# Kernel optimization log

Hardware: AMD Instinct MI355X
Metric: run time of the kernel (lower is better)

Reference implementation:

```python
import jax, jax.numpy as jnp
import numpy as np

N_X = 3
NE = 2048
Emin = 1.0
Emax = 100.0


def setup_inputs() -> dict:
    key = jax.random.key(0)
    k1, k2, k3, k4 = jax.random.split(key, 4)
    # log-spaced energy grid (MeV); code assumes E_grid[0] == Emin
    E_grid = jnp.logspace(np.log10(Emin), np.log10(Emax), NE, dtype=jnp.float32)
    # rates O(1), kernels small -> diagonally dominant per-step system, stable recursion
    R = 1.0 + jax.random.uniform(k1, (N_X, NE), dtype=jnp.float32)
    K = 1e-3 * jax.random.uniform(k2, (N_X, N_X, NE, NE), dtype=jnp.float32)
    S0 = jax.random.uniform(k3, (N_X,), dtype=jnp.float32)
    SC = jax.random.uniform(k4, (N_X, NE), dtype=jnp.float32)
    T = jnp.float32(0.01)
    return {"E_grid": E_grid, "R": R, "K": K, "S0": S0, "SC": SC, "T": T}


def _solve_cascade(E_grid, R, K, S0, SC, T):
    n_x, ne = R.shape
    dy = jnp.log(E_grid[-1] / Emin) / (ne - 1)

    src_last = S0 / R[:, -1]  # (N_X,) : S0[Xp] / R[Xp, -1]
    # boundary value at highest energy: FX_E0[X] = SC[X,-1]/R[X,-1] + sum_Xp K[X,Xp,-1,-1]*S0[Xp]/(R[Xp,-1]*R[X,-1])
    FX_E0 = SC[:, -1] / R[:, -1] + (K[:, :, -1, -1] @ src_last) / R[:, -1]
    F0 = jnp.zeros((n_x, ne), dtype=E_grid.dtype).at[:, -1].set(FX_E0)

    jidx = jnp.arange(ne)

    def step(F, i):
        Ki = K[:, :, i, :]  # (N_X, N_X, NE) slice at outer grid point i
        # trapezoid weights over j: dy*E[j] for i < j < NE-1, half-weight at j = NE-1, 0 elsewhere
        w = jnp.where((jidx > i) & (jidx < ne - 1), dy * E_grid, jnp.zeros((), E_grid.dtype))
        w = w.at[-1].set(0.5 * dy * E_grid[-1])
        # a[X] = SC[X,i] + sum_Xp,j Ki[X,Xp,j] * w[j] * F[Xp,j] + sum_Xp Ki[X,Xp,-1]*S0[Xp]/R[Xp,-1]
        a = SC[:, i] + jnp.einsum('xpj,pj->x', Ki, w * F) + Ki[:, :, -1] @ src_last
        # B[X,Xp] = -0.5*dy*E[i]*K[X,Xp,i,i] + R[X,i]*delta(X,Xp)
        B = -0.5 * dy * E_grid[i] * Ki[:, :, i] + jnp.diag(R[:, i])
        F = F.at[:, i].set(jnp.linalg.solve(B, a))
        return F, None

    idx = jnp.arange(ne - 2, -1, -1)  # backward sweep i = NE-2 ... 0
    F_grid, _ = jax.lax.scan(step, F0, idx)

    approx_zero = jnp.asarray(1e-200, F_grid.dtype)  # underflows to 0 in fp32, matching clamp intent
    F_grid = jnp.where(F_grid > approx_zero, F_grid, approx_zero)

    # sol: row 0 = E_grid, rows 1..N_X = spectra
    return jnp.concatenate([E_grid[None, :], F_grid], axis=0)


def reference(E_grid, R, K, S0, SC, T):
    return _solve_cascade(E_grid, R, K, S0, SC, T)
```

## Files before the change

### kernel.cpp

```cpp
#include <hip/hip_runtime.h>
#include <cstddef>
#include <cstdint>

#define NE 2048
#define NX 3
#define NROWS (NE - 1)
#define BS 64
#define BR (3 * BS)
#define NBLK 32
#define NPAIR 16


static __device__ __forceinline__ float dy_of(const float* E) {
    return logf(E[NE - 1] / E[0]) / (float)(NE - 1);
}

#define DOT4(a, b) ((a).x * (b).x + (a).y * (b).y + (a).z * (b).z + (a).w * (b).w)
#define FMA4(acc, s, b) { (acc).x += (s) * (b).x; (acc).y += (s) * (b).y; \
                          (acc).z += (s) * (b).z; (acc).w += (s) * (b).w; }

__global__ void k_init(const float* __restrict__ E, const float* __restrict__ R,
                       const float* __restrict__ K, const float* __restrict__ S0,
                       const float* __restrict__ SC,
                       float* __restrict__ out, float* __restrict__ wf,
                       float* __restrict__ acc) {
    int i = blockIdx.x * blockDim.x + threadIdx.x;
    if (i >= NE) return;
    const size_t PL = (size_t)NE * NE;
    float dy = dy_of(E);
    float wlast = 0.5f * dy * E[NE - 1];
    float srcl[NX], Fl[NX];
#pragma unroll
    for (int p = 0; p < NX; ++p) srcl[p] = S0[p] / R[p * NE + NE - 1];
#pragma unroll
    for (int x = 0; x < NX; ++x) {
        float s = SC[x * NE + NE - 1];
#pragma unroll
        for (int p = 0; p < NX; ++p)
            s += K[(size_t)(x * NX + p) * PL + (size_t)(NE - 1) * NE + (NE - 1)] * srcl[p];
        Fl[x] = s / R[x * NE + NE - 1];
    }
    out[i] = E[i];
    if (i == NE - 1) {
#pragma unroll
        for (int x = 0; x < NX; ++x) {
            out[(1 + x) * NE + i] = Fl[x] > 0.f ? Fl[x] : 0.f;
            wf[x * NE + i] = wlast * Fl[x];
            acc[x * NE + i] = 0.f;
        }
        return;
    }
#pragma unroll
    for (int x = 0; x < NX; ++x) {
        float s = SC[x * NE + i];
#pragma unroll
        for (int p = 0; p < NX; ++p)
            s += K[(size_t)(x * NX + p) * PL + (size_t)i * NE + (NE - 1)] *
                 (wlast * Fl[p] + srcl[p]);
        acc[x * NE + i] = s;
    }
}

__global__ __launch_bounds__(256) void k_tinv16(const float* __restrict__ E,
                                                const float* __restrict__ R,
                                                const float* __restrict__ K,
                                                float* __restrict__ Gs16) {
    __shared__ float4 Xs4[16][49];
    __shared__ float Kst[16][16][12];
    __shared__ float Binv[16][9];
    __shared__ float wloc[16];
    const size_t PL = (size_t)NE * NE;
    int sb = blockIdx.x;
    int i0 = sb * 16;
    int tid = threadIdx.x;
    float dy = dy_of(E);

    if (tid < 16) {
        int j = i0 + tid;
        wloc[tid] = (j < NE - 1) ? dy * E[j] : 0.f;
        int i = i0 + tid, ii = tid;
        float b00, b01, b02, b10, b11, b12, b20, b21, b22;
        if (i < NROWS) {
            float h = -0.5f * dy * E[i];
            size_t d = (size_t)i * NE + i;
            b00 = h * K[0 * PL + d] + R[0 * NE + i];
            b01 = h * K[1 * PL + d];
            b02 = h * K[2 * PL + d];
            b10 = h * K[3 * PL + d];
            b11 = h * K[4 * PL + d] + R[1 * NE + i];
            b12 = h * K[5 * PL + d];
            b20 = h * K[6 * PL + d];
            b21 = h * K[7 * PL + d];
            b22 = h * K[8 * PL + d] + R[2 * NE + i];
        } else {
            b00 = 1.f; b01 = 0.f; b02 = 0.f;
            b10 = 0.f; b11 = 1.f; b12 = 0.f;
            b20 = 0.f; b21 = 0.f; b22 = 1.f;
        }
        float C00 = b11 * b22 - b12 * b21;
        float C01 = -(b10 * b22 - b12 * b20);
        float C02 = b10 * b21 - b11 * b20;
        float C10 = -(b01 * b22 - b02 * b21);
        float C11 = b00 * b22 - b02 * b20;
        float C12 = -(b00 * b21 - b01 * b20);
        float C20 = b01 * b12 - b02 * b11;
        float C21 = -(b00 * b12 - b02 * b10);
        float C22 = b00 * b11 - b01 * b10;
        float inv = 1.f / (b00 * C00 + b01 * C01 + b02 * C02);
        Binv[ii][0] = C00 * inv; Binv[ii][1] = C10 * inv; Binv[ii][2] = C20 * inv;
        Binv[ii][3] = C01 * inv; Binv[ii][4] = C11 * inv; Binv[ii][5] = C21 * inv;
        Binv[ii][6] = C02 * inv; Binv[ii][7] = C12 * inv; Binv[ii][8] = C22 * inv;
    }
    __syncthreads();
    for (int q = tid; q < 16 * 16 * 9; q += 256) {
        int jj = q & 15;
        int ii = (q >> 4) & 15;
        int pair = q >> 8;
        Kst[ii][jj][4 * (pair / 3) + (pair % 3)] =
            K[(size_t)pair * PL + (size_t)(i0 + ii) * NE + (i0 + jj)] * wloc[jj];
    }
    __syncthreads();

    int cloc = tid >> 2, sub = tid & 3;
    if (cloc < 48) {
        for (int ii = 15; ii >= 0; --ii) {
            int i = i0 + ii;
            float v0 = 0.f, v1 = 0.f, v2 = 0.f;
            if (sub == 0) {
                v0 = (cloc == 0 * 16 + ii) ? 1.f : 0.f;
                v1 = (cloc == 1 * 16 + ii) ? 1.f : 0.f;
                v2 = (cloc == 2 * 16 + ii) ? 1.f : 0.f;
            }
            if (i < NROWS) {
                for (int jj = ii + 1 + sub; jj < 16; jj += 4) {
                    const float* kp = &Kst[ii][jj][0];
                    float4 k0 = *(const float4*)(kp);
                    float4 k1 = *(const float4*)(kp + 4);
                    float4 k2 = *(const float4*)(kp + 8);
                    float4 xv = Xs4[jj][cloc];
                    v0 += k0.x * xv.x + k0.y * xv.y + k0.z * xv.z;
                    v1 += k1.x * xv.x + k1.y * xv.y + k1.z * xv.z;
                    v2 += k2.x * xv.x + k2.y * xv.y + k2.z * xv.z;
                }
            }
            v0 += __shfl_xor(v0, 1); v0 += __shfl_xor(v0, 2);
            v1 += __shfl_xor(v1, 1); v1 += __shfl_xor(v1, 2);
            v2 += __shfl_xor(v2, 1); v2 += __shfl_xor(v2, 2);
            if (sub == 0) {
                float f0, f1, f2;
                if (i < NROWS) {
                    const float* bv = Binv[ii];
                    f0 = bv[0] * v0 + bv[1] * v1 + bv[2] * v2;
                    f1 = bv[3] * v0 + bv[4] * v1 + bv[5] * v2;
                    f2 = bv[6] * v0 + bv[7] * v1 + bv[8] * v2;
                } else {
                    f0 = v0; f1 = v1; f2 = v2;
                }
                Xs4[ii][cloc] = make_float4(f0, f1, f2, 0.f);
            }
            __builtin_amdgcn_wave_barrier();
        }
    }
    __syncthreads();
    float* Gb = Gs16 + (size_t)sb * 48 * 48;
    for (int t = tid; t < 48 * 48; t += 256) {
        int rp = t / 48, c = t % 48;
        int x = rp >> 4, ii = rp & 15;
        Gb[t] = ((const float*)&Xs4[ii][c])[x];
    }
}

__global__ __launch_bounds__(256) void k_merge48(const float* __restrict__ E,
                                                 const float* __restrict__ K,
                                                 const float* __restrict__ Gs16,
                                                 float* __restrict__ G32) {
    __shared__ float Ls[48][49], Bs[48][49], Ks[48][49], Ms[48][49];
    const size_t PL = (size_t)NE * NE;
    int q = blockIdx.x;
    int i0 = q * 32;
    int tid = threadIdx.x;
    float dy = dy_of(E);
    const float* GL = Gs16 + (size_t)(2 * q) * 2304;
    const float* GH = Gs16 + (size_t)(2 * q + 1) * 2304;
    for (int t = tid; t < 2304; t += 256) {
        int r = t / 48, c = t % 48;
        Ls[r][c] = GL[t];
        Bs[r][c] = GH[t];
        int x = r >> 4, ii = r & 15, p = c >> 4, jj = c & 15;
        int j = i0 + 16 + jj;
        float w = (j < NE - 1) ? dy * E[j] : 0.f;
        Ks[r][c] = w * K[(size_t)(x * 3 + p) * PL + (size_t)(i0 + ii) * NE + j];
    }
    __syncthreads();
    int tx = tid & 15, ty = tid >> 4;
    float m[3][3] = {};
    for (int k = 0; k < 48; ++k) {
        float a0 = Ks[ty * 3 + 0][k], a1 = Ks[ty * 3 + 1][k], a2 = Ks[ty * 3 + 2][k];
        float b0 = Bs[k][tx * 3 + 0], b1 = Bs[k][tx * 3 + 1], b2 = Bs[k][tx * 3 + 2];
        m[0][0] += a0 * b0; m[0][1] += a0 * b1; m[0][2] += a0 * b2;
        m[1][0] += a1 * b0; m[1][1] += a1 * b1; m[1][2] += a1 * b2;
        m[2][0] += a2 * b0; m[2][1] += a2 * b1; m[2][2] += a2 * b2;
    }
#pragma unroll
    for (int i = 0; i < 3; ++i)
#pragma unroll
        for (int j = 0; j < 3; ++j) Ms[ty * 3 + i][tx * 3 + j] = m[i][j];
    __syncthreads();
    float cc[3][3] = {};
    for (int k = 0; k < 48; ++k) {
        float a0 = Ls[ty * 3 + 0][k], a1 = Ls[ty * 3 + 1][k], a2 = Ls[ty * 3 + 2][k];
        float b0 = Ms[k][tx * 3 + 0], b1 = Ms[k][tx * 3 + 1], b2 = Ms[k][tx * 3 + 2];
        cc[0][0] += a0 * b0; cc[0][1] += a0 * b1; cc[0][2] += a0 * b2;
        cc[1][0] += a1 * b0; cc[1][1] += a1 * b1; cc[1][2] += a1 * b2;
        cc[2][0] += a2 * b0; cc[2][1] += a2 * b1; cc[2][2] += a2 * b2;
    }
    float* O = G32 + (size_t)q * 96 * 96;
    for (int t = tid; t < 2304; t += 256) {
        int r = t / 48, c = t % 48;
        int x = r >> 4, ii = r & 15, p = c >> 4, jj = c & 15;
        O[(size_t)(x * 32 + ii) * 96 + (p * 32 + jj)] = Ls[r][c];
        O[(size_t)(x * 32 + 16 + ii) * 96 + (p * 32 + 16 + jj)] = Bs[r][c];
        O[(size_t)(x * 32 + 16 + ii) * 96 + (p * 32 + jj)] = 0.f;
    }
#pragma unroll
    for (int i = 0; i < 3; ++i)
#pragma unroll
        for (int j = 0; j < 3; ++j) {
            int r = ty * 3 + i, c = tx * 3 + j;
            int x = r >> 4, ii = r & 15, p = c >> 4, jj = c & 15;
            O[(size_t)(x * 32 + ii) * 96 + (p * 32 + 16 + jj)] = cc[i][j];
        }
}

__global__ __launch_bounds__(256) void k_merge96(const float* __restrict__ E,
                                                 const float* __restrict__ K,
                                                 const float* __restrict__ G32,
                                                 float* __restrict__ G) {
    __shared__ float Bs[96][97], Kws[96][97], Ms[96][97];
    const size_t PL = (size_t)NE * NE;
    int b = blockIdx.x;
    int i0 = b * 64;
    int tid = threadIdx.x;
    float dy = dy_of(E);
    const float* GL = G32 + (size_t)(2 * b) * 9216;
    const float* GH = G32 + (size_t)(2 * b + 1) * 9216;
    for (int t = tid; t < 9216; t += 256) {
        int r = t / 96, k = t % 96;
        Bs[r][k] = GH[t];
        int x = r / 32, ii = r % 32, p = k / 32, jj = k % 32;
        int j = i0 + 32 + jj;
        float w = (j < NE - 1) ? dy * E[j] : 0.f;
        Kws[r][k] = w * K[(size_t)(x * 3 + p) * PL + (size_t)(i0 + ii) * NE + j];
    }
    __syncthreads();
    int tx = tid & 15, ty = tid >> 4;
    float m[6][6] = {};
    for (int k = 0; k < 96; ++k) {
        float a[6], bb[6];
#pragma unroll
        for (int i = 0; i < 6; ++i) a[i] = Kws[ty * 6 + i][k];
#pragma unroll
        for (int j = 0; j < 6; ++j) bb[j] = Bs[k][tx * 6 + j];
#pragma unroll
        for (int i = 0; i < 6; ++i)
#pragma unroll
            for (int j = 0; j < 6; ++j) m[i][j] += a[i] * bb[j];
    }
    __syncthreads();
#pragma unroll
    for (int i = 0; i < 6; ++i)
#pragma unroll
        for (int j = 0; j < 6; ++j) Ms[ty * 6 + i][tx * 6 + j] = m[i][j];
    __syncthreads();
    float cc[6][6] = {};
    for (int k = 0; k < 96; ++k) {
        float a[6], bb[6];
#pragma unroll
        for (int i = 0; i < 6; ++i) a[i] = GL[(size_t)(ty * 6 + i) * 96 + k];
#pragma unroll
        for (int j = 0; j < 6; ++j) bb[j] = Ms[k][tx * 6 + j];
#pragma unroll
        for (int i = 0; i < 6; ++i)
#pragma unroll
            for (int j = 0; j < 6; ++j) cc[i][j] += a[i] * bb[j];
    }
    float* O = G + (size_t)b * BR * BR;
    for (int t = tid; t < 9216; t += 256) {
        int r = t / 96, c = t % 96;
        int x = r / 32, er = r % 32, p = c / 32, ec = c % 32;
        O[(size_t)(x * 64 + er) * BR + (p * 64 + ec)] = GL[t];
        O[(size_t)(x * 64 + 32 + er) * BR + (p * 64 + 32 + ec)] = Bs[r][c];
        O[(size_t)(x * 64 + 32 + er) * BR + (p * 64 + ec)] = 0.f;
    }
#pragma unroll
    for (int i = 0; i < 6; ++i)
#pragma unroll
        for (int j = 0; j < 6; ++j) {
            int r = ty * 6 + i, c = tx * 6 + j;
            int x = r / 32, er = r % 32, p = c / 32, ec = c % 32;
            O[(size_t)(x * 64 + er) * BR + (p * 64 + 32 + ec)] = cc[i][j];
        }
}

__global__ __launch_bounds__(256) void k_gops1(const float* __restrict__ K,
                                               const float* __restrict__ G,
                                               float* __restrict__ ops1) {
    int s = blockIdx.x, ty_ = blockIdx.y, tz = blockIdx.z;
    int rt = tz / 3, ct = tz % 3;
    int t = ty_ + 1;
    float* O = ops1 + (size_t)(s * 3 + ty_) * BR * BR;
    int tid = threadIdx.x;
    if (s + t > NBLK - 1) {
        for (int q = tid; q < 64 * 64; q += 256)
            O[(size_t)(rt * 64 + q / 64) * BR + ct * 64 + (q % 64)] = 0.f;
        return;
    }
    const size_t PL = (size_t)NE * NE;
    const float* Ga = G + (size_t)s * BR * BR;
    int tgt0 = (s + t) * 64;
    int tx = tid & 15, ty = tid >> 4;
    int row0 = rt * 64 + ty * 4;
    int c0 = tx * 4;
    bool maskLast = (s + t == NBLK - 1) && (tx == 15);
    float4 acc0 = {0, 0, 0, 0}, acc1 = {0, 0, 0, 0};
    float4 acc2 = {0, 0, 0, 0}, acc3 = {0, 0, 0, 0};
    for (int k0 = 0; k0 < BR; k0 += 4) {
        int x = k0 >> 6;
        const float* Bb = K + (size_t)(x * 3 + ct) * PL +
                          (size_t)(s * 64 + (k0 & 63)) * NE + tgt0 + c0;
        float4 b0 = *(const float4*)(Bb);
        float4 b1 = *(const float4*)(Bb + NE);
        float4 b2 = *(const float4*)(Bb + 2 * NE);
        float4 b3 = *(const float4*)(Bb + 3 * NE);
        if (maskLast) { b0.w = 0.f; b1.w = 0.f; b2.w = 0.f; b3.w = 0.f; }
        float4 a0 = *(const float4*)(Ga + (size_t)(row0 + 0) * BR + k0);
        float4 a1 = *(const float4*)(Ga + (size_t)(row0 + 1) * BR + k0);
        float4 a2 = *(const float4*)(Ga + (size_t)(row0 + 2) * BR + k0);
        float4 a3 = *(const float4*)(Ga + (size_t)(row0 + 3) * BR + k0);
        FMA4(acc0, a0.x, b0); FMA4(acc0, a0.y, b1); FMA4(acc0, a0.z, b2); FMA4(acc0, a0.w, b3);
        FMA4(acc1, a1.x, b0); FMA4(acc1, a1.y, b1); FMA4(acc1, a1.z, b2); FMA4(acc1, a1.w, b3);
        FMA4(acc2, a2.x, b0); FMA4(acc2, a2.y, b1); FMA4(acc2, a2.z, b2); FMA4(acc2, a2.w, b3);
        FMA4(acc3, a3.x, b0); FMA4(acc3, a3.y, b1); FMA4(acc3, a3.z, b2); FMA4(acc3, a3.w, b3);
    }
    float* Ob = O + (size_t)row0 * BR + ct * 64 + c0;
    *(float4*)(Ob + 0 * BR) = acc0;
    *(float4*)(Ob + 1 * BR) = acc1;
    *(float4*)(Ob + 2 * BR) = acc2;
    *(float4*)(Ob + 3 * BR) = acc3;
}

__global__ __launch_bounds__(256) void k_gops2(const float* __restrict__ E,
                                               const float* __restrict__ G,
                                               const float* __restrict__ ops1,
                                               float* __restrict__ pr) {
    int m = blockIdx.x, w = blockIdx.y, tz = blockIdx.z;
    int rt = tz / 3, ct = tz % 3;
    int A = 2 * m, C = 2 * m + 1;
    int tid = threadIdx.x;
    float dy = dy_of(E);
    const float* Asrc = ops1 + (size_t)(A * 3 + 0) * BR * BR;
    const float* Bsrc = (w == 0) ? (G + (size_t)C * BR * BR)
                                 : (ops1 + (size_t)(C * 3 + (w - 1)) * BR * BR);
    const float* Dsrc = (w == 0) ? nullptr : (ops1 + (size_t)(A * 3 + w) * BR * BR);
    float* O = pr + (size_t)(m * 3 + w) * BR * BR;
    int tx = tid & 15, ty = tid >> 4;
    int row0 = rt * 64 + ty * 4;
    int c0 = ct * 64 + tx * 4;
    float4 acc0 = {0, 0, 0, 0}, acc1 = {0, 0, 0, 0};
    float4 acc2 = {0, 0, 0, 0}, acc3 = {0, 0, 0, 0};
    for (int k0 = 0; k0 < BR; k0 += 4) {
        int e0 = C * 64 + (k0 & 63);
        float w0 = (e0 + 0 < NROWS) ? dy * E[e0 + 0] : 0.f;
        float w1 = (e0 + 1 < NROWS) ? dy * E[e0 + 1] : 0.f;
        float w2 = (e0 + 2 < NROWS) ? dy * E[e0 + 2] : 0.f;
        float w3 = (e0 + 3 < NROWS) ? dy * E[e0 + 3] : 0.f;
        const float* Bb = Bsrc + (size_t)k0 * BR + c0;
        float4 b0 = *(const float4*)(Bb + 0 * BR);
        float4 b1 = *(const float4*)(Bb + 1 * BR);
        float4 b2 = *(const float4*)(Bb + 2 * BR);
        float4 b3 = *(const float4*)(Bb + 3 * BR);
        b0.x *= w0; b0.y *= w0; b0.z *= w0; b0.w *= w0;
        b1.x *= w1; b1.y *= w1; b1.z *= w1; b1.w *= w1;
        b2.x *= w2; b2.y *= w2; b2.z *= w2; b2.w *= w2;
        b3.x *= w3; b3.y *= w3; b3.z *= w3; b3.w *= w3;
        float4 a0 = *(const float4*)(Asrc + (size_t)(row0 + 0) * BR + k0);
        float4 a1 = *(const float4*)(Asrc + (size_t)(row0 + 1) * BR + k0);
        float4 a2 = *(const float4*)(Asrc + (size_t)(row0 + 2) * BR + k0);
        float4 a3 = *(const float4*)(Asrc + (size_t)(row0 + 3) * BR + k0);
        FMA4(acc0, a0.x, b0); FMA4(acc0, a0.y, b1); FMA4(acc0, a0.z, b2); FMA4(acc0, a0.w, b3);
        FMA4(acc1, a1.x, b0); FMA4(acc1, a1.y, b1); FMA4(acc1, a1.z, b2); FMA4(acc1, a1.w, b3);
        FMA4(acc2, a2.x, b0); FMA4(acc2, a2.y, b1); FMA4(acc2, a2.z, b2); FMA4(acc2, a2.w, b3);
        FMA4(acc3, a3.x, b0); FMA4(acc3, a3.y, b1); FMA4(acc3, a3.z, b2); FMA4(acc3, a3.w, b3);
    }
    float* Ob = O + (size_t)row0 * BR + c0;
    if (Dsrc) {
        const float* Db = Dsrc + (size_t)row0 * BR + c0;
        float4 d0 = *(const float4*)(Db + 0 * BR);
        float4 d1 = *(const float4*)(Db + 1 * BR);
        float4 d2 = *(const float4*)(Db + 2 * BR);
        float4 d3 = *(const float4*)(Db + 3 * BR);
        acc0.x += d0.x; acc0.y += d0.y; acc0.z += d0.z; acc0.w += d0.w;
        acc1.x += d1.x; acc1.y += d1.y; acc1.z += d1.z; acc1.w += d1.w;
        acc2.x += d2.x; acc2.y += d2.y; acc2.z += d2.z; acc2.w += d2.w;
        acc3.x += d3.x; acc3.y += d3.y; acc3.z += d3.z; acc3.w += d3.w;
    }
    *(float4*)(Ob + 0 * BR) = acc0;
    *(float4*)(Ob + 1 * BR) = acc1;
    *(float4*)(Ob + 2 * BR) = acc2;
    *(float4*)(Ob + 3 * BR) = acc3;
}

__global__ __launch_bounds__(512) void k_pair2(const float* __restrict__ E,
                                               const float* __restrict__ K,
                                               const float* __restrict__ G,
                                               const float* __restrict__ ops1,
                                               const float* __restrict__ pr,
                                               float* __restrict__ acc,
                                               float* __restrict__ wf,
                                               float* __restrict__ out,
                                               int m, int hasV) {
    const size_t PL = (size_t)NE * NE;
    int A = 2 * m, C = 2 * m + 1;
    int tid = threadIdx.x;
    int bid = blockIdx.x;
    int lane = tid & 63, wv = tid >> 6;

    if (bid >= 12) {
        int jbase = (2 * m + 2) * BS;
        int row = (bid - 12) * 8 + wv;
        int j1 = jbase + lane, j2 = j1 + BS;
        float w10 = wf[0 * NE + j1], w11 = wf[1 * NE + j1], w12 = wf[2 * NE + j1];
        float w20 = 0.f, w21 = 0.f, w22 = 0.f;
        if (j2 < NROWS) {
            w20 = wf[0 * NE + j2]; w21 = wf[1 * NE + j2]; w22 = wf[2 * NE + j2];
        }
        const float* Kb1 = K + (size_t)row * NE + j1;
        const float* Kb2 = K + (size_t)row * NE + j2;
        float s0 = Kb1[0 * PL] * w10 + Kb1[1 * PL] * w11 + Kb1[2 * PL] * w12
                 + Kb2[0 * PL] * w20 + Kb2[1 * PL] * w21 + Kb2[2 * PL] * w22;
        float s1 = Kb1[3 * PL] * w10 + Kb1[4 * PL] * w11 + Kb1[5 * PL] * w12
                 + Kb2[3 * PL] * w20 + Kb2[4 * PL] * w21 + Kb2[5 * PL] * w22;
        float s2 = Kb1[6 * PL] * w10 + Kb1[7 * PL] * w11 + Kb1[8 * PL] * w12
                 + Kb2[6 * PL] * w20 + Kb2[7 * PL] * w21 + Kb2[8 * PL] * w22;
#pragma unroll
        for (int d = 32; d; d >>= 1) {
            s0 += __shfl_xor(s0, d);
            s1 += __shfl_xor(s1, d);
            s2 += __shfl_xor(s2, d);
        }
        if (lane == 0) {
            atomicAdd(&acc[0 * NE + row], s0);
            atomicAdd(&acc[1 * NE + row], s1);
            atomicAdd(&acc[2 * NE + row], s2);
        }
        return;
    }

    __shared__ float4 vec4[4][BR / 4];
    float dy = dy_of(E);
    if (tid < BR) {
        int sp = tid >> 6, e = tid & 63;
        ((float*)vec4[0])[tid] = __hip_atomic_load(&acc[sp * NE + C * BS + e],
                                     __ATOMIC_RELAXED, __HIP_MEMORY_SCOPE_AGENT);
        ((float*)vec4[1])[tid] = __hip_atomic_load(&acc[sp * NE + A * BS + e],
                                     __ATOMIC_RELAXED, __HIP_MEMORY_SCOPE_AGENT);
        ((float*)vec4[2])[tid] = hasV ? wf[sp * NE + (2 * m + 2) * BS + e] : 0.f;
        ((float*)vec4[3])[tid] = hasV ? wf[sp * NE + (2 * m + 3) * BS + e] : 0.f;
    }
    __syncthreads();

    int rloc = tid >> 4, sub = tid & 15;
    bool isC = (bid < 6);
    int rbase = (isC ? bid : bid - 6) * 32;
    int row = rbase + rloc;
    int blk = isC ? C : A;

    const float4* m0 = (const float4*)(G + ((size_t)blk * BR + row) * BR) + sub * 3;
    const float4 *m1, *m2, *m3 = nullptr;
    const float4 *x0, *x1, *x2, *x3 = nullptr;
    if (isC) {
        m1 = (const float4*)(ops1 + ((size_t)(C * 3 + 0) * BR + row) * BR) + sub * 3;
        m2 = (const float4*)(ops1 + ((size_t)(C * 3 + 1) * BR + row) * BR) + sub * 3;
        x0 = vec4[0] + sub * 3; x1 = vec4[2] + sub * 3; x2 = vec4[3] + sub * 3;
    } else {
        m1 = (const float4*)(pr + ((size_t)(m * 3 + 0) * BR + row) * BR) + sub * 3;
        m2 = (const float4*)(pr + ((size_t)(m * 3 + 1) * BR + row) * BR) + sub * 3;
        m3 = (const float4*)(pr + ((size_t)(m * 3 + 2) * BR + row) * BR) + sub * 3;
        x0 = vec4[1] + sub * 3; x1 = vec4[0] + sub * 3;
        x2 = vec4[2] + sub * 3; x3 = vec4[3] + sub * 3;
    }
    float s = 0.f;
#pragma unroll
    for (int q = 0; q < 3; ++q) s += DOT4(m0[q], x0[q]);
    if (hasV || !isC) {
#pragma unroll
        for (int q = 0; q < 3; ++q) s += DOT4(m1[q], x1[q]);
    }
    if (hasV) {
#pragma unroll
        for (int q = 0; q < 3; ++q) s += DOT4(m2[q], x2[q]);
        if (!isC) {
#pragma unroll
            for (int q = 0; q < 3; ++q) s += DOT4(m3[q], x3[q]);
        }
    }
    s += __shfl_xor(s, 1); s += __shfl_xor(s, 2);
    s += __shfl_xor(s, 4); s += __shfl_xor(s, 8);
    if (sub == 0) {
        int x = row >> 6, ii = row & 63;
        int i = blk * BS + ii;
        if (i < NROWS) {
            out[(1 + x) * NE + i] = s > 0.f ? s : 0.f;
            wf[x * NE + i] = dy * E[i] * s;
        }
    }
}

extern "C" void kernel_launch(void* const* d_in, const int* in_sizes, int n_in,
                              void* d_out, int out_size, void* d_ws, size_t ws_size,
                              hipStream_t stream) {
    const float* E = (const float*)d_in[0];
    const float* R = (const float*)d_in[1];
    const float* K = (const float*)d_in[2];
    const float* S0 = (const float*)d_in[3];
    const float* SC = (const float*)d_in[4];
    float* out = (float*)d_out;
    float* wf = (float*)d_ws;
    float* acc = wf + NX * NE;
    float* G = acc + NX * NE;
    float* ops1 = G + (size_t)NBLK * BR * BR;
    float* pr = ops1 + (size_t)NBLK * 3 * BR * BR;
    float* Gs16 = pr + (size_t)NPAIR * 3 * BR * BR;
    float* G32 = Gs16 + (size_t)128 * 48 * 48;

    k_init<<<(NE + 255) / 256, 256, 0, stream>>>(E, R, K, S0, SC, out, wf, acc);
    k_tinv16<<<128, 256, 0, stream>>>(E, R, K, Gs16);
    k_merge48<<<64, 256, 0, stream>>>(E, K, Gs16, G32);
    k_merge96<<<32, 256, 0, stream>>>(E, K, G32, G);
    k_gops1<<<dim3(NBLK, 3, 9), 256, 0, stream>>>(K, G, ops1);
    k_gops2<<<dim3(NPAIR, 3, 9), 256, 0, stream>>>(E, G, ops1, pr);

    for (int m = NPAIR - 1; m >= 0; --m) {
        int nFar = (m < NPAIR - 1) ? m * 16 : 0;
        int hasV = (m < NPAIR - 1) ? 1 : 0;
        k_pair2<<<12 + nFar, 512, 0, stream>>>(E, K, G, ops1, pr, acc, wf, out,
                                               m, hasV);
    }
}
```

Measured before the change: 248.9 us.

## Fuse init into tinv16 launch and split merge96 into two parallel GEMM kernels

New measurement: 223.7 us (median of 2 runs). -10.1%, faster.

```diff
diff --git a/kernel.cpp b/kernel.cpp
--- a/kernel.cpp
+++ b/kernel.cpp
@@ -6,7 +6,7 @@
 #define NX 3
 #define NROWS (NE - 1)
 #define BS 64
-#define BR (3 * BS)
+#define BR 192
 #define NBLK 32
 #define NPAIR 16
 
@@ -19,61 +19,62 @@
 #define FMA4(acc, s, b) { (acc).x += (s) * (b).x; (acc).y += (s) * (b).y; \
                           (acc).z += (s) * (b).z; (acc).w += (s) * (b).w; }
 
-__global__ void k_init(const float* __restrict__ E, const float* __restrict__ R,
-                       const float* __restrict__ K, const float* __restrict__ S0,
-                       const float* __restrict__ SC,
-                       float* __restrict__ out, float* __restrict__ wf,
-                       float* __restrict__ acc) {
-    int i = blockIdx.x * blockDim.x + threadIdx.x;
-    if (i >= NE) return;
+__global__ __launch_bounds__(256) void k_boot(const float* __restrict__ E,
+                                              const float* __restrict__ R,
+                                              const float* __restrict__ K,
+                                              const float* __restrict__ S0,
+                                              const float* __restrict__ SC,
+                                              float* __restrict__ out,
+                                              float* __restrict__ wf,
+                                              float* __restrict__ acc,
+                                              float* __restrict__ Gs16) {
     const size_t PL = (size_t)NE * NE;
+    int tid = threadIdx.x;
     float dy = dy_of(E);
-    float wlast = 0.5f * dy * E[NE - 1];
-    float srcl[NX], Fl[NX];
-#pragma unroll
-    for (int p = 0; p < NX; ++p) srcl[p] = S0[p] / R[p * NE + NE - 1];
-#pragma unroll
-    for (int x = 0; x < NX; ++x) {
-        float s = SC[x * NE + NE - 1];
-#pragma unroll
-        for (int p = 0; p < NX; ++p)
-            s += K[(size_t)(x * NX + p) * PL + (size_t)(NE - 1) * NE + (NE - 1)] * srcl[p];
-        Fl[x] = s / R[x * NE + NE - 1];
-    }
-    out[i] = E[i];
-    if (i == NE - 1) {
+
+    if (blockIdx.x < 8) {
+        int i = blockIdx.x * 256 + tid;
+        if (i >= NE) return;
+        float wlast = 0.5f * dy * E[NE - 1];
+        float srcl[NX], Fl[NX];
+#pragma unroll
+        for (int p = 0; p < NX; ++p) srcl[p] = S0[p] / R[p * NE + NE - 1];
 #pragma unroll
         for (int x = 0; x < NX; ++x) {
-            out[(1 + x) * NE + i] = Fl[x] > 0.f ? Fl[x] : 0.f;
-            wf[x * NE + i] = wlast * Fl[x];
-            acc[x * NE + i] = 0.f;
+            float s = SC[x * NE + NE - 1];
+#pragma unroll
+            for (int p = 0; p < NX; ++p)
+                s += K[(size_t)(x * NX + p) * PL + (size_t)(NE - 1) * NE + (NE - 1)] * srcl[p];
+            Fl[x] = s / R[x * NE + NE - 1];
+        }
+        out[i] = E[i];
+        if (i == NE - 1) {
+#pragma unroll
+            for (int x = 0; x < NX; ++x) {
+                out[(1 + x) * NE + i] = Fl[x] > 0.f ? Fl[x] : 0.f;
+                wf[x * NE + i] = wlast * Fl[x];
+                acc[x * NE + i] = 0.f;
+            }
+            return;
+        }
+#pragma unroll
+        for (int x = 0; x < NX; ++x) {
+            float s = SC[x * NE + i];
+#pragma unroll
+            for (int p = 0; p < NX; ++p)
+                s += K[(size_t)(x * NX + p) * PL + (size_t)i * NE + (NE - 1)] *
+                     (wlast * Fl[p] + srcl[p]);
+            acc[x * NE + i] = s;
         }
         return;
     }
-#pragma unroll
-    for (int x = 0; x < NX; ++x) {
-        float s = SC[x * NE + i];
-#pragma unroll
-        for (int p = 0; p < NX; ++p)
-            s += K[(size_t)(x * NX + p) * PL + (size_t)i * NE + (NE - 1)] *
-                 (wlast * Fl[p] + srcl[p]);
-        acc[x * NE + i] = s;
-    }
-}
-
-__global__ __launch_bounds__(256) void k_tinv16(const float* __restrict__ E,
-                                                const float* __restrict__ R,
-                                                const float* __restrict__ K,
-                                                float* __restrict__ Gs16) {
+
     __shared__ float4 Xs4[16][49];
     __shared__ float Kst[16][16][12];
     __shared__ float Binv[16][9];
     __shared__ float wloc[16];
-    const size_t PL = (size_t)NE * NE;
-    int sb = blockIdx.x;
+    int sb = blockIdx.x - 8;
     int i0 = sb * 16;
-    int tid = threadIdx.x;
-    float dy = dy_of(E);
 
     if (tid < 16) {
         int j = i0 + tid;
@@ -232,74 +233,97 @@
         }
 }
 
-__global__ __launch_bounds__(256) void k_merge96(const float* __restrict__ E,
-                                                 const float* __restrict__ K,
-                                                 const float* __restrict__ G32,
-                                                 float* __restrict__ G) {
-    __shared__ float Bs[96][97], Kws[96][97], Ms[96][97];
+__global__ __launch_bounds__(256) void k_mA32(const float* __restrict__ E,
+                                              const float* __restrict__ K,
+                                              const float* __restrict__ srcG,
+                                              float* __restrict__ M) {
     const size_t PL = (size_t)NE * NE;
-    int b = blockIdx.x;
-    int i0 = b * 64;
-    int tid = threadIdx.x;
+    const int h = 96, he = 32;
+    int mg = blockIdx.x, tz = blockIdx.y;
+    int tr = tz / 3, tc = tz % 3;
+    int tid = threadIdx.x;
+    int tx = tid & 15, ty = tid >> 4;
+    int i0 = mg * 64;
+    int row0 = tr * 32 + ty * 2;
+    int c0 = tc * 32 + tx * 2;
     float dy = dy_of(E);
-    const float* GL = G32 + (size_t)(2 * b) * 9216;
-    const float* GH = G32 + (size_t)(2 * b + 1) * 9216;
-    for (int t = tid; t < 9216; t += 256) {
-        int r = t / 96, k = t % 96;
-        Bs[r][k] = GH[t];
-        int x = r / 32, ii = r % 32, p = k / 32, jj = k % 32;
-        int j = i0 + 32 + jj;
-        float w = (j < NE - 1) ? dy * E[j] : 0.f;
-        Kws[r][k] = w * K[(size_t)(x * 3 + p) * PL + (size_t)(i0 + ii) * NE + j];
-    }
-    __syncthreads();
+    const float* GH = srcG + (size_t)(2 * mg + 1) * h * h;
+    int xr = row0 / he, er = row0 % he;
+    float2 acc0 = {0, 0}, acc1 = {0, 0};
+    for (int k0 = 0; k0 < h; k0 += 4) {
+        int p = k0 / he, ek = k0 % he;
+        int j0 = i0 + he + ek;
+        float w0 = (j0 + 0 < NE - 1) ? dy * E[j0 + 0] : 0.f;
+        float w1 = (j0 + 1 < NE - 1) ? dy * E[j0 + 1] : 0.f;
+        float w2 = (j0 + 2 < NE - 1) ? dy * E[j0 + 2] : 0.f;
+        float w3 = (j0 + 3 < NE - 1) ? dy * E[j0 + 3] : 0.f;
+        const float* Kp = K + (size_t)(xr * 3 + p) * PL + (size_t)(i0 + er) * NE + j0;
+        float4 a0 = *(const float4*)(Kp);
+        float4 a1 = *(const float4*)(Kp + NE);
+        a0.x *= w0; a0.y *= w1; a0.z *= w2; a0.w *= w3;
+        a1.x *= w0; a1.y *= w1; a1.z *= w2; a1.w *= w3;
+        float2 b0 = *(const float2*)(GH + (size_t)(k0 + 0) * h + c0);
+        float2 b1 = *(const float2*)(GH + (size_t)(k0 + 1) * h + c0);
+        float2 b2 = *(const float2*)(GH + (size_t)(k0 + 2) * h + c0);
+        float2 b3 = *(const float2*)(GH + (size_t)(k0 + 3) * h + c0);
+        acc0.x += a0.x * b0.x + a0.y * b1.x + a0.z * b2.x + a0.w * b3.x;
+        acc0.y += a0.x * b0.y + a0.y * b1.y + a0.z * b2.y + a0.w * b3.y;
+        acc1.x += a1.x * b0.x + a1.y * b1.x + a1.z * b2.x + a1.w * b3.x;
+        acc1.y += a1.x * b0.y + a1.y * b1.y + a1.z * b2.y + a1.w * b3.y;
+    }
+    float* Ob = M + (size_t)mg * h * h + (size_t)row0 * h + c0;
+    *(float2*)(Ob) = acc0;
+    *(float2*)(Ob + h) = acc1;
+}
+
+__global__ __launch_bounds__(256) void k_mB32(const float* __restrict__ srcG,
+                                              const float* __restrict__ M,
+                                              float* __restrict__ dst) {
+    const int h = 96, n = 192;
+    int mg = blockIdx.x, tz = blockIdx.y;
+    int tr = tz / 6, tc = tz % 6;
+    int tid = threadIdx.x;
     int tx = tid & 15, ty = tid >> 4;
-    float m[6][6] = {};
-    for (int k = 0; k < 96; ++k) {
-        float a[6], bb[6];
-#pragma unroll
-        for (int i = 0; i < 6; ++i) a[i] = Kws[ty * 6 + i][k];
-#pragma unroll
-        for (int j = 0; j < 6; ++j) bb[j] = Bs[k][tx * 6 + j];
-#pragma unroll
-        for (int i = 0; i < 6; ++i)
-#pragma unroll
-            for (int j = 0; j < 6; ++j) m[i][j] += a[i] * bb[j];
-    }
-    __syncthreads();
-#pragma unroll
-    for (int i = 0; i < 6; ++i)
-#pragma unroll
-        for (int j = 0; j < 6; ++j) Ms[ty * 6 + i][tx * 6 + j] = m[i][j];
-    __syncthreads();
-    float cc[6][6] = {};
-    for (int k = 0; k < 96; ++k) {
-        float a[6], bb[6];
-#pragma unroll
-        for (int i = 0; i < 6; ++i) a[i] = GL[(size_t)(ty * 6 + i) * 96 + k];
-#pragma unroll
-        for (int j = 0; j < 6; ++j) bb[j] = Ms[k][tx * 6 + j];
-#pragma unroll
-        for (int i = 0; i < 6; ++i)
-#pragma unroll
-            for (int j = 0; j < 6; ++j) cc[i][j] += a[i] * bb[j];
-    }
-    float* O = G + (size_t)b * BR * BR;
-    for (int t = tid; t < 9216; t += 256) {
-        int r = t / 96, c = t % 96;
-        int x = r / 32, er = r % 32, p = c / 32, ec = c % 32;
-        O[(size_t)(x * 64 + er) * BR + (p * 64 + ec)] = GL[t];
-        O[(size_t)(x * 64 + 32 + er) * BR + (p * 64 + 32 + ec)] = Bs[r][c];
-        O[(size_t)(x * 64 + 32 + er) * BR + (p * 64 + ec)] = 0.f;
-    }
-#pragma unroll
-    for (int i = 0; i < 6; ++i)
-#pragma unroll
-        for (int j = 0; j < 6; ++j) {
-            int r = ty * 6 + i, c = tx * 6 + j;
-            int x = r / 32, er = r % 32, p = c / 32, ec = c % 32;
-            O[(size_t)(x * 64 + er) * BR + (p * 64 + 32 + ec)] = cc[i][j];
-        }
+    int row0 = tr * 32 + ty * 2;
+    int c0 = tc * 32 + tx * 2;
+    const float* GL = srcG + (size_t)(2 * mg) * h * h;
+    const float* GH = srcG + (size_t)(2 * mg + 1) * h * h;
+    const float* Mb = M + (size_t)mg * h * h;
+    float* O = dst + (size_t)mg * n * n;
+    int xr = row0 / 64, e2r = row0 % 64;
+    int xc = c0 / 64, e2c = c0 % 64;
+    bool rtop = e2r < 32, ctop = e2c < 32;
+    if (rtop && ctop) {
+        const float* S = GL + (size_t)(xr * 32 + e2r) * h + (xc * 32 + e2c);
+        *(float2*)(O + (size_t)row0 * n + c0) = *(const float2*)(S);
+        *(float2*)(O + (size_t)(row0 + 1) * n + c0) = *(const float2*)(S + h);
+    } else if (!rtop && !ctop) {
+        const float* S = GH + (size_t)(xr * 32 + e2r - 32) * h + (xc * 32 + e2c - 32);
+        *(float2*)(O + (size_t)row0 * n + c0) = *(const float2*)(S);
+        *(float2*)(O + (size_t)(row0 + 1) * n + c0) = *(const float2*)(S + h);
+    } else if (!rtop && ctop) {
+        float2 z = {0, 0};
+        *(float2*)(O + (size_t)row0 * n + c0) = z;
+        *(float2*)(O + (size_t)(row0 + 1) * n + c0) = z;
+    } else {
+        const float* Ar = GL + (size_t)(xr * 32 + e2r) * h;
+        int cm = xc * 32 + (e2c - 32);
+        float2 acc0 = {0, 0}, acc1 = {0, 0};
+        for (int k0 = 0; k0 < h; k0 += 4) {
+            float4 a0 = *(const float4*)(Ar + k0);
+            float4 a1 = *(const float4*)(Ar + h + k0);
+            float2 b0 = *(const float2*)(Mb + (size_t)(k0 + 0) * h + cm);
+            float2 b1 = *(const float2*)(Mb + (size_t)(k0 + 1) * h + cm);
+            float2 b2 = *(const float2*)(Mb + (size_t)(k0 + 2) * h + cm);
+            float2 b3 = *(const float2*)(Mb + (size_t)(k0 + 3) * h + cm);
+            acc0.x += a0.x * b0.x + a0.y * b1.x + a0.z * b2.x + a0.w * b3.x;
+            acc0.y += a0.x * b0.y + a0.y * b1.y + a0.z * b2.y + a0.w * b3.y;
+            acc1.x += a1.x * b0.x + a1.y * b1.x + a1.z * b2.x + a1.w * b3.x;
+            acc1.y += a1.x * b0.y + a1.y * b1.y + a1.z * b2.y + a1.w * b3.y;
+        }
+        *(float2*)(O + (size_t)row0 * n + c0) = acc0;
+        *(float2*)(O + (size_t)(row0 + 1) * n + c0) = acc1;
+    }
 }
 
 __global__ __launch_bounds__(256) void k_gops1(const float* __restrict__ K,
@@ -526,24 +550,25 @@
     const float* SC = (const float*)d_in[4];
     float* out = (float*)d_out;
     float* wf = (float*)d_ws;
-    float* acc = wf + NX * NE;
-    float* G = acc + NX * NE;
-    float* ops1 = G + (size_t)NBLK * BR * BR;
+    float* acc = wf + 6144;
+    float* Gs16 = acc + 6144;
+    float* L1 = Gs16 + (size_t)128 * 48 * 48;
+    float* L2 = L1 + (size_t)64 * 96 * 96;
+    float* ops1 = L2 + (size_t)32 * 192 * 192;
     float* pr = ops1 + (size_t)NBLK * 3 * BR * BR;
-    float* Gs16 = pr + (size_t)NPAIR * 3 * BR * BR;
-    float* G32 = Gs16 + (size_t)128 * 48 * 48;
-
-    k_init<<<(NE + 255) / 256, 256, 0, stream>>>(E, R, K, S0, SC, out, wf, acc);
-    k_tinv16<<<128, 256, 0, stream>>>(E, R, K, Gs16);
-    k_merge48<<<64, 256, 0, stream>>>(E, K, Gs16, G32);
-    k_merge96<<<32, 256, 0, stream>>>(E, K, G32, G);
-    k_gops1<<<dim3(NBLK, 3, 9), 256, 0, stream>>>(K, G, ops1);
-    k_gops2<<<dim3(NPAIR, 3, 9), 256, 0, stream>>>(E, G, ops1, pr);
+    float* Mtmp = pr + (size_t)NPAIR * 3 * BR * BR;
+
+    k_boot<<<136, 256, 0, stream>>>(E, R, K, S0, SC, out, wf, acc, Gs16);
+    k_merge48<<<64, 256, 0, stream>>>(E, K, Gs16, L1);
+    k_mA32<<<dim3(32, 9), 256, 0, stream>>>(E, K, L1, Mtmp);
+    k_mB32<<<dim3(32, 36), 256, 0, stream>>>(L1, Mtmp, L2);
+    k_gops1<<<dim3(NBLK, 3, 9), 256, 0, stream>>>(K, L2, ops1);
+    k_gops2<<<dim3(NPAIR, 3, 9), 256, 0, stream>>>(E, L2, ops1, pr);
 
     for (int m = NPAIR - 1; m >= 0; --m) {
         int nFar = (m < NPAIR - 1) ? m * 16 : 0;
         int hasV = (m < NPAIR - 1) ? 1 : 0;
-        k_pair2<<<12 + nFar, 512, 0, stream>>>(E, K, G, ops1, pr, acc, wf, out,
+        k_pair2<<<12 + nFar, 512, 0, stream>>>(E, K, L2, ops1, pr, acc, wf, out,
                                                m, hasV);
     }
 }
```
